# Kernel optimization log

Hardware: AMD Instinct MI355X
Metric: run time of the kernel (lower is better)

The kernel has to match this reference:

```python
import jax, jax.numpy as jnp
import numpy as np

B, V, C, H, W, D = 1, 3, 32, 320, 320, 32


def setup_inputs() -> dict:
    key = jax.random.key(0)
    ks = jax.random.split(key, 14)
    feats = jax.random.normal(ks[0], (B, V, C, H, W), jnp.float32)
    # Valid pinhole projections: P = [[K @ [R|t]], [0,0,0,1]], identity rotation,
    # horizontal baselines sized so the warp stays mostly in-image over the depth range.
    K = np.array([[400.0, 0.0, W / 2.0], [0.0, 400.0, H / 2.0], [0.0, 0.0, 1.0]])
    mats = []
    for tx in (0.0, 100.0, -100.0):
        Rt = np.eye(4)
        Rt[0, 3] = tx
        P = np.eye(4)
        P[:3, :4] = K @ Rt[:3, :4]
        mats.append(P)
    proj = jnp.asarray(np.broadcast_to(np.stack(mats)[None], (B, V, 4, 4)).copy(), jnp.float32)
    planes = jnp.linspace(425.0, 935.0, D, dtype=jnp.float32)
    depth_values = jnp.broadcast_to(planes[None, :, None, None], (B, D, H, W)).astype(jnp.float32)
    s = 0.05  # small init so exp(reg_cost) stays well-scaled
    W0 = s * jax.random.normal(ks[1], (8, C, 3, 3), jnp.float32)
    Ws1 = s * jax.random.normal(ks[2], (8, 8, 3, 3), jnp.float32)
    W1 = s * jax.random.normal(ks[3], (16, 8, 3, 3), jnp.float32)
    Ws2 = s * jax.random.normal(ks[4], (16, 16, 3, 3), jnp.float32)
    W2 = s * jax.random.normal(ks[5], (32, 16, 3, 3), jnp.float32)
    Ws3 = s * jax.random.normal(ks[6], (32, 32, 3, 3), jnp.float32)
    W3 = s * jax.random.normal(ks[7], (64, 32, 3, 3), jnp.float32)
    Ws4 = s * jax.random.normal(ks[8], (64, 64, 3, 3), jnp.float32)
    U4 = s * jax.random.normal(ks[9], (32, 64, 1, 1), jnp.float32)
    U3 = s * jax.random.normal(ks[10], (16, 32, 1, 1), jnp.float32)
    U2 = s * jax.random.normal(ks[11], (8, 16, 1, 1), jnp.float32)
    Wout = s * jax.random.normal(ks[12], (1, 8, 3, 3), jnp.float32)
    return dict(feats=feats, proj=proj, depth_values=depth_values, W0=W0, Ws1=Ws1,
                W1=W1, Ws2=Ws2, W2=W2, Ws3=Ws3, W3=W3, Ws4=Ws4, U4=U4, U3=U3, U2=U2, Wout=Wout)


def _conv(x, w, stride=1):
    return jax.lax.conv_general_dilated(x, w, (stride, stride), 'SAME',
                                        dimension_numbers=('NCHW', 'OIHW', 'NCHW'))


def _up2(x):
    return jnp.repeat(jnp.repeat(x, 2, axis=2), 2, axis=3)


def _bilinear(img, x, y):
    # img [C,H,W]; x,y [N] pixel coords; zero padding, align_corners semantics
    Cc, Hh, Ww = img.shape
    x0 = jnp.floor(x)
    y0 = jnp.floor(y)
    wx = x - x0
    wy = y - y0

    def tap(xi, yi):
        valid = ((xi >= 0) & (xi <= Ww - 1) & (yi >= 0) & (yi <= Hh - 1)).astype(img.dtype)
        xc = jnp.clip(xi, 0, Ww - 1).astype(jnp.int32)
        yc = jnp.clip(yi, 0, Hh - 1).astype(jnp.int32)
        return img[:, yc, xc] * valid  # [C,N]

    return (tap(x0, y0) * (1 - wx) * (1 - wy) + tap(x0 + 1, y0) * wx * (1 - wy)
            + tap(x0, y0 + 1) * (1 - wx) * wy + tap(x0 + 1, y0 + 1) * wx * wy)


def _forward(feats, proj, depth_values, W0, Ws1, W1, Ws2, W2, Ws3, W3, Ws4, U4, U3, U2, Wout):
    Bn, Vn, Cn, Hn, Wn = feats.shape
    Dn = depth_values.shape[1]
    N = Hn * Wn
    relu = jax.nn.relu
    ref = feats[:, 0]
    ref_sq = ref * ref
    # Precompute per-src-view rotated pixel rays and translations.
    inv_ref = jnp.linalg.inv(proj[:, 0])                       # [B,4,4]
    rel = jnp.einsum('bvij,bjk->bvik', proj[:, 1:], inv_ref)   # [B,V-1,4,4]
    rot, trans = rel[:, :, :3, :3], rel[:, :, :3, 3]
    ys, xs = jnp.meshgrid(jnp.arange(Hn), jnp.arange(Wn), indexing='ij')
    pix = jnp.stack([xs.ravel(), ys.ravel(), jnp.ones(N)], 0).astype(feats.dtype)  # [3,N]
    rot_pix = jnp.einsum('bvij,jn->bvin', rot, pix)            # [B,V-1,3,N]

    def regularize(x, s1, s2, s3, s4):
        c1 = relu(_conv(x, W0) + _conv(s1, Ws1))
        c2 = relu(_conv(c1, W1, 2) + _conv(s2, Ws2))
        c3 = relu(_conv(c2, W2, 2) + _conv(s3, Ws3))
        c4 = relu(_conv(c3, W3, 2) + _conv(s4, Ws4))
        u3 = c3 + _up2(_conv(c4, U4))
        u2 = c2 + _up2(_conv(u3, U3))
        u1 = c1 + _up2(_conv(u2, U2))
        return _conv(u1, Wout), c1, c2, c3, c4

    def step(carry, depth_slice):  # depth_slice [B,H,W]
        s1, s2, s3, s4, exp_sum, depth_img, max_prob = carry
        vol_sum, vol_sq = ref, ref_sq
        dflat = depth_slice.reshape(Bn, 1, N)
        for v in range(Vn - 1):
            xyz = rot_pix[:, v] * dflat + trans[:, v, :, None]   # [B,3,N]
            px = xyz[:, 0] / xyz[:, 2]
            py = xyz[:, 1] / xyz[:, 2]
            warped = jax.vmap(_bilinear)(feats[:, v + 1], px, py).reshape(Bn, Cn, Hn, Wn)
            vol_sum = vol_sum + warped
            vol_sq = vol_sq + warped * warped
        variance = vol_sq / Vn - (vol_sum / Vn) ** 2
        cost, s1, s2, s3, s4 = regularize(variance, s1, s2, s3, s4)
        prob = jnp.exp(cost)                                     # [B,1,H,W]
        max_prob = jnp.maximum(max_prob, prob)                   # == flag*prob + (1-flag)*max
        depth_img = depth_img + depth_slice[:, None] * prob
        exp_sum = exp_sum + prob
        return (s1, s2, s3, s4, exp_sum, depth_img, max_prob), None

    z = lambda c, h, w: jnp.zeros((Bn, c, h, w), feats.dtype)
    init = (z(8, Hn, Wn), z(16, Hn // 2, Wn // 2), z(32, Hn // 4, Wn // 4), z(64, Hn // 8, Wn // 8),
            z(1, Hn, Wn), z(1, Hn, Wn), z(1, Hn, Wn))
    carry, _ = jax.lax.scan(step, init, jnp.moveaxis(depth_values, 1, 0))
    _, _, _, _, exp_sum, depth_img, max_prob = carry
    es = exp_sum + 1e-10
    depth_map = (depth_img / es)[:, 0]
    prob_map = (max_prob / es)[:, 0]
    return jnp.stack([depth_map, prob_map], axis=1)  # [B,2,H,W]


def reference(feats, proj, depth_values, W0, Ws1, W1, Ws2, W2, Ws3, W3, Ws4, U4, U3, U2, Wout):
    return _forward(feats, proj, depth_values, W0, Ws1, W1, Ws2, W2, Ws3, W3, Ws4, U4, U3, U2, Wout)
```

## Files before the change

### kernel.cpp

```cpp
#include <hip/hip_runtime.h>
#include <hip/hip_bf16.h>
#include <math.h>

#define HH 320
#define WW 320
#define NP (HH*WW)
#define CC 32
#define DD 32

#define H2 160
#define W2 160
#define N2 (H2*W2)
#define H4 80
#define W4 80
#define N4 (H4*W4)
#define H8 40
#define W8 40
#define N8 (H8*W8)

#define HALO 18
#define NHALO (HALO*HALO)

#define C1SZ (8*NP)
#define C2SZ (16*N2)
#define C3SZ (32*N4)
#define C4SZ (64*N8)

#define SMEM_FLOATS (32*36 + 16*100 + 8*NHALO)

#define OFF_REL   0
#define OFF_C1R   64
#define OFF_C2R   (OFF_C1R + 5*C1SZ)
#define OFF_C3R   (OFF_C2R + 4*C2SZ)
#define OFF_C4R   (OFF_C3R + 3*C3SZ)
#define OFF_ESUM  (OFF_C4R + 2*C4SZ)
#define OFF_DIMG  (OFF_ESUM + NP)
#define OFF_MAXP  (OFF_DIMG + NP)
#define OFF_END   (OFF_MAXP + NP)

__global__ void k_prep(const float* __restrict__ proj, float* __restrict__ rel) {
    if (threadIdx.x != 0 || blockIdx.x != 0) return;
    double a[4][8];
    for (int i = 0; i < 4; i++)
        for (int j = 0; j < 4; j++) {
            a[i][j] = (double)proj[i*4 + j];
            a[i][j+4] = (i == j) ? 1.0 : 0.0;
        }
    for (int c = 0; c < 4; c++) {
        int pv = c; double best = fabs(a[c][c]);
        for (int r = c+1; r < 4; r++) {
            double v = fabs(a[r][c]);
            if (v > best) { best = v; pv = r; }
        }
        if (pv != c)
            for (int j = 0; j < 8; j++) { double t = a[c][j]; a[c][j] = a[pv][j]; a[pv][j] = t; }
        double inv = 1.0 / a[c][c];
        for (int j = 0; j < 8; j++) a[c][j] *= inv;
        for (int r = 0; r < 4; r++) if (r != c) {
            double f = a[r][c];
            for (int j = 0; j < 8; j++) a[r][j] -= f * a[c][j];
        }
    }
    for (int v = 1; v < 3; v++) {
        const float* P = proj + v*16;
        double rm[4][4];
        for (int i = 0; i < 4; i++)
            for (int j = 0; j < 4; j++) {
                double s = 0.0;
                for (int k = 0; k < 4; k++) s += (double)P[i*4 + k] * a[k][j+4];
                rm[i][j] = s;
            }
        float* o = rel + (v-1)*12;
        o[0]=(float)rm[0][0]; o[1]=(float)rm[0][1]; o[2]=(float)rm[0][2];
        o[3]=(float)rm[1][0]; o[4]=(float)rm[1][1]; o[5]=(float)rm[1][2];
        o[6]=(float)rm[2][0]; o[7]=(float)rm[2][1]; o[8]=(float)rm[2][2];
        o[9]=(float)rm[0][3]; o[10]=(float)rm[1][3]; o[11]=(float)rm[2][3];
    }
}


__device__ void stageA(int blk, int d,
        const float* __restrict__ feats, const float* __restrict__ rel,
        const float* __restrict__ depthv, const float* __restrict__ c1r,
        const float* __restrict__ W0, const float* __restrict__ Ws1,
        float* buf) {
    const float* dslice = depthv + (size_t)d * NP;
    const float* s1 = c1r + (size_t)((d+4)%5) * C1SZ;
    float* c1out = (float*)c1r + (size_t)(d%5) * C1SZ;

    int bx = blk % 20, by = blk / 20;
    int ox0 = bx*16, oy0 = by*16;

    const float* f1 = feats + CC*NP;
    const float* f2 = feats + 2*CC*NP;
    const float inv3 = 1.0f / 3.0f;

    int opx = threadIdx.x & 15, opy = threadIdx.x >> 4;
    int obase = opy*HALO + opx;
    int outp = (oy0 + opy)*WW + ox0 + opx;

    float acc[8];
#pragma unroll
    for (int o = 0; o < 8; o++) acc[o] = 0.0f;

    for (int chunk = 0; chunk < 4; chunk++) {
        int cbase = chunk*8;
        for (int hp = threadIdx.x; hp < NHALO; hp += 256) {
            int hy = hp / HALO, hx = hp - hy*HALO;
            int gy = oy0 + hy - 1, gx = ox0 + hx - 1;
            if (gy < 0 || gy >= HH || gx < 0 || gx >= WW) {
#pragma unroll
                for (int c = 0; c < 8; c++) buf[c*NHALO + hp] = 0.0f;
            } else {
                int p = gy*WW + gx;
                float depth = dslice[p];
                float fx = (float)gx, fy = (float)gy;
                int offs[8]; float wts[8];
#pragma unroll
                for (int v = 0; v < 2; v++) {
                    const float* r = rel + v*12;
                    float X = (r[0]*fx + r[1]*fy + r[2]) * depth + r[9];
                    float Y = (r[3]*fx + r[4]*fy + r[5]) * depth + r[10];
                    float Z = (r[6]*fx + r[7]*fy + r[8]) * depth + r[11];
                    float iz = 1.0f / Z;
                    float px = X * iz, py = Y * iz;
                    float x0f = floorf(px), y0f = floorf(py);
                    float wx = px - x0f, wy = py - y0f;
                    int x0 = (int)x0f, y0 = (int)y0f;
#pragma unroll
                    for (int t = 0; t < 4; t++) {
                        int xi = x0 + (t & 1), yi = y0 + (t >> 1);
                        float wgt = ((t & 1) ? wx : 1.0f - wx) * ((t >> 1) ? wy : 1.0f - wy);
                        bool valid = (xi >= 0) && (xi <= WW-1) && (yi >= 0) && (yi <= HH-1);
                        int xc = min(max(xi, 0), WW-1);
                        int yc = min(max(yi, 0), HH-1);
                        offs[v*4 + t] = yc*WW + xc;
                        wts[v*4 + t] = valid ? wgt : 0.0f;
                    }
                }
#pragma unroll
                for (int c = 0; c < 8; c++) {
                    int cg = cbase + c;
                    float rv = feats[cg*NP + p];
                    float sum = rv, sq = rv * rv;
                    const float* b1 = f1 + cg*NP;
                    float t1 = b1[offs[0]]*wts[0] + b1[offs[1]]*wts[1] + b1[offs[2]]*wts[2] + b1[offs[3]]*wts[3];
                    const float* b2 = f2 + cg*NP;
                    float t2 = b2[offs[4]]*wts[4] + b2[offs[5]]*wts[5] + b2[offs[6]]*wts[6] + b2[offs[7]]*wts[7];
                    sum += t1 + t2;
                    sq  += t1*t1 + t2*t2;
                    float m = sum * inv3;
                    buf[c*NHALO + hp] = sq * inv3 - m*m;
                }
            }
        }
        __syncthreads();
        for (int ci = 0; ci < 8; ci++) {
            float t[9];
#pragma unroll
            for (int ky = 0; ky < 3; ky++)
#pragma unroll
                for (int kx = 0; kx < 3; kx++) t[ky*3+kx] = buf[ci*NHALO + obase + ky*HALO + kx];
#pragma unroll
            for (int o = 0; o < 8; o++) {
                const float* w = W0 + (o*32 + cbase + ci)*9;
                float a = acc[o];
#pragma unroll
                for (int k = 0; k < 9; k++) a += t[k] * w[k];
                acc[o] = a;
            }
        }
        __syncthreads();
    }

    for (int hp = threadIdx.x; hp < NHALO; hp += 256) {
        int hy = hp / HALO, hx = hp - hy*HALO;
        int gy = oy0 + hy - 1, gx = ox0 + hx - 1;
        bool v = (gy >= 0) && (gy < HH) && (gx >= 0) && (gx < WW);
        int p = v ? gy*WW + gx : 0;
#pragma unroll
        for (int c = 0; c < 8; c++) buf[c*NHALO + hp] = v ? s1[c*NP + p] : 0.0f;
    }
    __syncthreads();
    for (int ci = 0; ci < 8; ci++) {
        float t[9];
#pragma unroll
        for (int ky = 0; ky < 3; ky++)
#pragma unroll
            for (int kx = 0; kx < 3; kx++) t[ky*3+kx] = buf[ci*NHALO + obase + ky*HALO + kx];
#pragma unroll
        for (int o = 0; o < 8; o++) {
            const float* w = Ws1 + (o*8 + ci)*9;
            float a = acc[o];
#pragma unroll
            for (int k = 0; k < 9; k++) a += t[k] * w[k];
            acc[o] = a;
        }
    }
#pragma unroll
    for (int o = 0; o < 8; o++) c1out[o*NP + outp] = fmaxf(acc[o], 0.0f);
}

__device__ void stageB(int blk, int d,
        const float* __restrict__ c1r, const float* __restrict__ c2r_,
        const float* __restrict__ W1, const float* __restrict__ Ws2) {
    const float* c1 = c1r + (size_t)(d%5) * C1SZ;
    const float* s2 = c2r_ + (size_t)((d+3)%4) * C2SZ;
    float* c2 = (float*)c2r_ + (size_t)(d%4) * C2SZ;
    int p = (blk % 100)*256 + threadIdx.x;
    if (p >= N2) return;
    int og = blk / 100;
    int y = p / W2, x = p - y*W2;
    int offsA[9]; float mskA[9];
#pragma unroll
    for (int k = 0; k < 9; k++) {
        int yy = 2*y + k/3, xx = 2*x + k%3;
        bool v = (yy < HH) && (xx < WW);
        offsA[k] = v ? yy*WW + xx : 0;
        mskA[k] = v ? 1.0f : 0.0f;
    }
    int offsB[9]; float mskB[9];
#pragma unroll
    for (int k = 0; k < 9; k++) {
        int yy = y + k/3 - 1, xx = x + k%3 - 1;
        bool v = (yy >= 0) && (yy < H2) && (xx >= 0) && (xx < W2);
        offsB[k] = v ? yy*W2 + xx : 0;
        mskB[k] = v ? 1.0f : 0.0f;
    }
    float acc[4];
#pragma unroll
    for (int o = 0; o < 4; o++) acc[o] = 0.0f;
    for (int ci = 0; ci < 8; ci++) {
        const float* b = c1 + ci*NP;
        float t[9];
#pragma unroll
        for (int k = 0; k < 9; k++) t[k] = b[offsA[k]] * mskA[k];
#pragma unroll
        for (int o = 0; o < 4; o++) {
            const float* w = W1 + ((og*4 + o)*8 + ci)*9;
            float a = acc[o];
#pragma unroll
            for (int k = 0; k < 9; k++) a += t[k] * w[k];
            acc[o] = a;
        }
    }
    for (int ci = 0; ci < 16; ci++) {
        const float* b = s2 + ci*N2;
        float t[9];
#pragma unroll
        for (int k = 0; k < 9; k++) t[k] = b[offsB[k]] * mskB[k];
#pragma unroll
        for (int o = 0; o < 4; o++) {
            const float* w = Ws2 + ((og*4 + o)*16 + ci)*9;
            float a = acc[o];
#pragma unroll
            for (int k = 0; k < 9; k++) a += t[k] * w[k];
            acc[o] = a;
        }
    }
#pragma unroll
    for (int o = 0; o < 4; o++) c2[(og*4 + o)*N2 + p] = fmaxf(acc[o], 0.0f);
}

__device__ void stageC(int blk, int d,
        const float* __restrict__ c2r_, const float* __restrict__ c3r_,
        const float* __restrict__ W2w, const float* __restrict__ Ws3) {
    const float* c2 = c2r_ + (size_t)(d%4) * C2SZ;
    const float* s3 = c3r_ + (size_t)((d+2)%3) * C3SZ;
    float* c3 = (float*)c3r_ + (size_t)(d%3) * C3SZ;
    int p = (blk % 25)*256 + threadIdx.x;
    if (p >= N4) return;
    int og = blk / 25;
    int y = p / W4, x = p - y*W4;
    int offsA[9]; float mskA[9];
#pragma unroll
    for (int k = 0; k < 9; k++) {
        int yy = 2*y + k/3, xx = 2*x + k%3;
        bool v = (yy < H2) && (xx < W2);
        offsA[k] = v ? yy*W2 + xx : 0;
        mskA[k] = v ? 1.0f : 0.0f;
    }
    int offsB[9]; float mskB[9];
#pragma unroll
    for (int k = 0; k < 9; k++) {
        int yy = y + k/3 - 1, xx = x + k%3 - 1;
        bool v = (yy >= 0) && (yy < H4) && (xx >= 0) && (xx < W4);
        offsB[k] = v ? yy*W4 + xx : 0;
        mskB[k] = v ? 1.0f : 0.0f;
    }
    float acc[4];
#pragma unroll
    for (int o = 0; o < 4; o++) acc[o] = 0.0f;
    for (int ci = 0; ci < 16; ci++) {
        const float* b = c2 + ci*N2;
        float t[9];
#pragma unroll
        for (int k = 0; k < 9; k++) t[k] = b[offsA[k]] * mskA[k];
#pragma unroll
        for (int o = 0; o < 4; o++) {
            const float* w = W2w + ((og*4 + o)*16 + ci)*9;
            float a = acc[o];
#pragma unroll
            for (int k = 0; k < 9; k++) a += t[k] * w[k];
            acc[o] = a;
        }
    }
    for (int ci = 0; ci < 32; ci++) {
        const float* b = s3 + ci*N4;
        float t[9];
#pragma unroll
        for (int k = 0; k < 9; k++) t[k] = b[offsB[k]] * mskB[k];
#pragma unroll
        for (int o = 0; o < 4; o++) {
            const float* w = Ws3 + ((og*4 + o)*32 + ci)*9;
            float a = acc[o];
#pragma unroll
            for (int k = 0; k < 9; k++) a += t[k] * w[k];
            acc[o] = a;
        }
    }
#pragma unroll
    for (int o = 0; o < 4; o++) c3[(og*4 + o)*N4 + p] = fmaxf(acc[o], 0.0f);
}

__device__ void stageD(int blk, int d,
        const float* __restrict__ c3r_, const float* __restrict__ c4r_,
        const float* __restrict__ W3w, const float* __restrict__ Ws4) {
    const float* c3 = c3r_ + (size_t)(d%3) * C3SZ;
    const float* s4 = c4r_ + (size_t)((d+1)%2) * C4SZ;
    float* c4 = (float*)c4r_ + (size_t)(d%2) * C4SZ;
    int p = (blk % 7)*256 + threadIdx.x;
    if (p >= N8) return;
    int og = blk / 7;
    int y = p / W8, x = p - y*W8;
    int offsA[9]; float mskA[9];
#pragma unroll
    for (int k = 0; k < 9; k++) {
        int yy = 2*y + k/3, xx = 2*x + k%3;
        bool v = (yy < H4) && (xx < W4);
        offsA[k] = v ? yy*W4 + xx : 0;
        mskA[k] = v ? 1.0f : 0.0f;
    }
    int offsB[9]; float mskB[9];
#pragma unroll
    for (int k = 0; k < 9; k++) {
        int yy = y + k/3 - 1, xx = x + k%3 - 1;
        bool v = (yy >= 0) && (yy < H8) && (xx >= 0) && (xx < W8);
        offsB[k] = v ? yy*W8 + xx : 0;
        mskB[k] = v ? 1.0f : 0.0f;
    }
    float acc[4];
#pragma unroll
    for (int o = 0; o < 4; o++) acc[o] = 0.0f;
    for (int ci = 0; ci < 32; ci++) {
        const float* b = c3 + ci*N4;
        float t[9];
#pragma unroll
        for (int k = 0; k < 9; k++) t[k] = b[offsA[k]] * mskA[k];
#pragma unroll
        for (int o = 0; o < 4; o++) {
            const float* w = W3w + ((og*4 + o)*32 + ci)*9;
            float a = acc[o];
#pragma unroll
            for (int k = 0; k < 9; k++) a += t[k] * w[k];
            acc[o] = a;
        }
    }
    for (int ci = 0; ci < 64; ci++) {
        const float* b = s4 + ci*N8;
        float t[9];
#pragma unroll
        for (int k = 0; k < 9; k++) t[k] = b[offsB[k]] * mskB[k];
#pragma unroll
        for (int o = 0; o < 4; o++) {
            const float* w = Ws4 + ((og*4 + o)*64 + ci)*9;
            float a = acc[o];
#pragma unroll
            for (int k = 0; k < 9; k++) a += t[k] * w[k];
            acc[o] = a;
        }
    }
#pragma unroll
    for (int o = 0; o < 4; o++) c4[(og*4 + o)*N8 + p] = fmaxf(acc[o], 0.0f);
}

__device__ void stageU(int blk, int d,
        const float* __restrict__ c1r, const float* __restrict__ c2r_,
        const float* __restrict__ c3r_, const float* __restrict__ c4r_,
        const float* __restrict__ U4, const float* __restrict__ U3,
        const float* __restrict__ U2, const float* __restrict__ Wout,
        const float* __restrict__ depthv,
        float* __restrict__ exp_sum, float* __restrict__ depth_img,
        float* __restrict__ max_prob, float* smem) {
    const float* c1 = c1r + (size_t)(d%5) * C1SZ;
    const float* c2 = c2r_ + (size_t)(d%4) * C2SZ;
    const float* c3 = c3r_ + (size_t)(d%3) * C3SZ;
    const float* c4 = c4r_ + (size_t)(d%2) * C4SZ;
    const float* dslice = depthv + (size_t)d * NP;
    float* u3s = smem;
    float* u2s = smem + 32*36;
    float* u1s = smem + 32*36 + 16*100;

    int bx = blk % 20, by = blk / 20;
    int ox0 = bx*16, oy0 = by*16;
    int qy0 = (oy0 >> 2) - 1, qx0 = (ox0 >> 2) - 1;
    int hy0 = (oy0 >> 1) - 1, hx0 = (ox0 >> 1) - 1;

    for (int i = threadIdx.x; i < 32*36; i += 256) {
        int ch = i / 36, pp = i - ch*36;
        int y4 = qy0 + pp/6, x4 = qx0 + pp%6;
        int y4c = min(max(y4, 0), H4-1), x4c = min(max(x4, 0), W4-1);
        int pl = (y4c >> 1)*W8 + (x4c >> 1);
        const float* w = U4 + ch*64;
        float s = c3[ch*N4 + y4c*W4 + x4c];
#pragma unroll 8
        for (int ci = 0; ci < 64; ci++) s += c4[ci*N8 + pl] * w[ci];
        u3s[ch*36 + pp] = s;
    }
    __syncthreads();
    for (int i = threadIdx.x; i < 16*100; i += 256) {
        int ch = i / 100, pp = i - ch*100;
        int y2 = hy0 + pp/10, x2 = hx0 + pp%10;
        int y2c = min(max(y2, 0), H2-1), x2c = min(max(x2, 0), W2-1);
        int ly = (y2c >> 1) - qy0, lx = (x2c >> 1) - qx0;
        const float* w = U3 + ch*32;
        float s = c2[ch*N2 + y2c*W2 + x2c];
#pragma unroll 8
        for (int ci = 0; ci < 32; ci++) s += u3s[ci*36 + ly*6 + lx] * w[ci];
        u2s[ch*100 + pp] = s;
    }
    __syncthreads();
    for (int i = threadIdx.x; i < 8*NHALO; i += 256) {
        int ch = i / NHALO, pp = i - ch*NHALO;
        int gy = oy0 + pp/HALO - 1, gx = ox0 + pp%HALO - 1;
        float s = 0.0f;
        if (gy >= 0 && gy < HH && gx >= 0 && gx < WW) {
            int ly = (gy >> 1) - hy0, lx = (gx >> 1) - hx0;
            const float* w = U2 + ch*16;
            s = c1[ch*NP + gy*WW + gx];
#pragma unroll
            for (int ci = 0; ci < 16; ci++) s += u2s[ci*100 + ly*10 + lx] * w[ci];
        }
        u1s[ch*NHALO + pp] = s;
    }
    __syncthreads();
    int px = threadIdx.x & 15, py = threadIdx.x >> 4;
    int base = py*HALO + px;
    float cost = 0.0f;
#pragma unroll
    for (int ci = 0; ci < 8; ci++) {
        const float* w = Wout + ci*9;
#pragma unroll
        for (int ky = 0; ky < 3; ky++)
#pragma unroll
            for (int kx = 0; kx < 3; kx++)
                cost += u1s[ci*NHALO + base + ky*HALO + kx] * w[ky*3 + kx];
    }
    int p = (oy0 + py)*WW + ox0 + px;
    float prob = expf(cost);
    exp_sum[p] += prob;
    depth_img[p] += dslice[p] * prob;
    max_prob[p] = fmaxf(max_prob[p], prob);
}

__global__ __launch_bounds__(256) void k_uber(
        int t,
        const float* __restrict__ feats, const float* __restrict__ rel,
        const float* __restrict__ depthv,
        const float* __restrict__ W0, const float* __restrict__ Ws1,
        const float* __restrict__ W1, const float* __restrict__ Ws2,
        const float* __restrict__ W2w, const float* __restrict__ Ws3,
        const float* __restrict__ W3w, const float* __restrict__ Ws4,
        const float* __restrict__ U4, const float* __restrict__ U3,
        const float* __restrict__ U2, const float* __restrict__ Wout,
        float* __restrict__ c1r, float* __restrict__ c2r,
        float* __restrict__ c3r, float* __restrict__ c4r,
        float* __restrict__ esum, float* __restrict__ dimg,
        float* __restrict__ maxp) {
    __shared__ float smem[SMEM_FLOATS];
    int b = blockIdx.x;
    if (b < 400) {
        int d = t;
        if (d < DD) stageA(b, d, feats, rel, depthv, c1r, W0, Ws1, smem);
    } else if (b < 800) {
        int d = t - 1;
        if (d >= 0 && d < DD) stageB(b - 400, d, c1r, c2r, W1, Ws2);
    } else if (b < 1000) {
        int d = t - 2;
        if (d >= 0 && d < DD) stageC(b - 800, d, c2r, c3r, W2w, Ws3);
    } else if (b < 1112) {
        int d = t - 3;
        if (d >= 0 && d < DD) stageD(b - 1000, d, c3r, c4r, W3w, Ws4);
    } else {
        int d = t - 4;
        if (d >= 0 && d < DD)
            stageU(b - 1112, d, c1r, c2r, c3r, c4r, U4, U3, U2, Wout, depthv,
                   esum, dimg, maxp, smem);
    }
}

__global__ __launch_bounds__(256) void k_final(
        const float* __restrict__ exp_sum, const float* __restrict__ depth_img,
        const float* __restrict__ max_prob, float* __restrict__ out) {
    int p = blockIdx.x*256 + threadIdx.x;
    if (p >= NP) return;
    float es = exp_sum[p] + 1e-10f;
    out[p] = depth_img[p] / es;
    out[NP + p] = max_prob[p] / es;
}

extern "C" void kernel_launch(void* const* d_in, const int* in_sizes, int n_in,
                              void* d_out, int out_size, void* d_ws, size_t ws_size,
                              hipStream_t stream) {
    const float* feats = (const float*)d_in[0];
    const float* proj  = (const float*)d_in[1];
    const float* depthv= (const float*)d_in[2];
    const float* W0  = (const float*)d_in[3];
    const float* Ws1 = (const float*)d_in[4];
    const float* W1  = (const float*)d_in[5];
    const float* Ws2 = (const float*)d_in[6];
    const float* W2w = (const float*)d_in[7];
    const float* Ws3 = (const float*)d_in[8];
    const float* W3w = (const float*)d_in[9];
    const float* Ws4 = (const float*)d_in[10];
    const float* U4  = (const float*)d_in[11];
    const float* U3  = (const float*)d_in[12];
    const float* U2  = (const float*)d_in[13];
    const float* Wout= (const float*)d_in[14];

    float* ws = (float*)d_ws;
    float* rel  = ws + OFF_REL;
    float* c1r  = ws + OFF_C1R;
    float* c2r  = ws + OFF_C2R;
    float* c3r  = ws + OFF_C3R;
    float* c4r  = ws + OFF_C4R;
    float* esum = ws + OFF_ESUM;
    float* dimg = ws + OFF_DIMG;
    float* maxp = ws + OFF_MAXP;

    hipMemsetAsync(c1r, 0, (size_t)(OFF_END - OFF_C1R) * sizeof(float), stream);
    k_prep<<<1, 1, 0, stream>>>(proj, rel);

    for (int t = 0; t < DD + 4; t++) {
        k_uber<<<dim3(1512), 256, 0, stream>>>(t, feats, rel, depthv,
            W0, Ws1, W1, Ws2, W2w, Ws3, W3w, Ws4, U4, U3, U2, Wout,
            c1r, c2r, c3r, c4r, esum, dimg, maxp);
    }
    k_final<<<dim3(400), 256, 0, stream>>>(esum, dimg, maxp, (float*)d_out);
}
```

Baseline: 2.994 ms.

## Convert features to fp16 channels-last and retile all stages to NHWC with 128-thread blocks

Precomputes a channels-last fp16 copy of the input features so each bilinear tap loads 8 channels in one vector load instead of strided fp32 gathers. All intermediate activation ring buffers switch to pixel-major NHWC layout with float4 loads and stores. Blocks shrink to 128 threads over 16x8 tiles, which doubles the grid, and smem is padded to avoid bank conflicts. The fp16 features add rounding error to the variance cost volume, and the different reduction order may shift results slightly.

```diff
diff --git a/kernel.cpp b/kernel.cpp
--- a/kernel.cpp
+++ b/kernel.cpp
@@ -1,5 +1,6 @@
 #include <hip/hip_runtime.h>
 #include <hip/hip_bf16.h>
+#include <hip/hip_fp16.h>
 #include <math.h>
 
 #define HH 320
@@ -7,7 +8,6 @@
 #define NP (HH*WW)
 #define CC 32
 #define DD 32
-
 #define H2 160
 #define W2 160
 #define N2 (H2*W2)
@@ -18,25 +18,55 @@
 #define W8 40
 #define N8 (H8*W8)
 
-#define HALO 18
-#define NHALO (HALO*HALO)
+#define AHW 18
+#define AHH 10
+#define ANH (AHW*AHH)
+#define ABUF_STRIDE 184
+
+#define U3_PX 24
+#define U3_STRIDE 33
+#define U2_PX 60
+#define U2_STRIDE 17
+#define U1_PX 180
+#define U1_STRIDE 9
+
+#define SMEM_FLOATS (U3_PX*U3_STRIDE + U2_PX*U2_STRIDE + U1_PX*U1_STRIDE)
 
 #define C1SZ (8*NP)
 #define C2SZ (16*N2)
 #define C3SZ (32*N4)
 #define C4SZ (64*N8)
 
-#define SMEM_FLOATS (32*36 + 16*100 + 8*NHALO)
-
-#define OFF_REL   0
-#define OFF_C1R   64
-#define OFF_C2R   (OFF_C1R + 5*C1SZ)
-#define OFF_C3R   (OFF_C2R + 4*C2SZ)
-#define OFF_C4R   (OFF_C3R + 3*C3SZ)
-#define OFF_ESUM  (OFF_C4R + 2*C4SZ)
-#define OFF_DIMG  (OFF_ESUM + NP)
-#define OFF_MAXP  (OFF_DIMG + NP)
-#define OFF_END   (OFF_MAXP + NP)
+#define OFF_REL  0
+#define OFF_FH   64
+#define FH_FLOATS (3*NP*32/2)
+#define OFF_C1R  (OFF_FH + FH_FLOATS)
+#define OFF_C2R  (OFF_C1R + 5*C1SZ)
+#define OFF_C3R  (OFF_C2R + 4*C2SZ)
+#define OFF_C4R  (OFF_C3R + 3*C3SZ)
+#define OFF_ESUM (OFF_C4R + 2*C4SZ)
+#define OFF_DIMG (OFF_ESUM + NP)
+#define OFF_MAXP (OFF_DIMG + NP)
+#define OFF_END  (OFF_MAXP + NP)
+
+#define A_END 800
+#define B_END 1600
+#define C_END 2000
+#define D_END 2208
+#define TOT_BLK 3008
+
+__device__ __forceinline__ void load8h(const __half* b, float o[8]) {
+    float4 f = *reinterpret_cast<const float4*>(b);
+    const __half2* h = reinterpret_cast<const __half2*>(&f);
+#pragma unroll
+    for (int j = 0; j < 4; j++) { float2 t = __half22float2(h[j]); o[2*j] = t.x; o[2*j+1] = t.y; }
+}
+__device__ __forceinline__ void load8f(const float* b, float o[8]) {
+    float4 x = reinterpret_cast<const float4*>(b)[0];
+    float4 y = reinterpret_cast<const float4*>(b)[1];
+    o[0]=x.x; o[1]=x.y; o[2]=x.z; o[3]=x.w; o[4]=y.x; o[5]=y.y; o[6]=y.z; o[7]=y.w;
+}
+__device__ __forceinline__ void load16f(const float* b, float o[16]) { load8f(b,o); load8f(b+8,o+8); }
 
 __global__ void k_prep(const float* __restrict__ proj, float* __restrict__ rel) {
     if (threadIdx.x != 0 || blockIdx.x != 0) return;
@@ -78,44 +108,48 @@
     }
 }
 
+__global__ __launch_bounds__(256) void k_tofp16(const float* __restrict__ feats,
+                                                __half* __restrict__ fh) {
+    int i = blockIdx.x*256 + threadIdx.x;
+    if (i >= 3*NP) return;
+    int v = i / NP, p = i - v*NP;
+    const float* src = feats + (size_t)v*CC*NP + p;
+    union { __half h[32]; float4 f4[4]; } u;
+#pragma unroll
+    for (int c = 0; c < 32; c++) u.h[c] = __float2half(src[(size_t)c*NP]);
+    float4* dst = (float4*)(fh + (size_t)i*32);
+#pragma unroll
+    for (int q = 0; q < 4; q++) dst[q] = u.f4[q];
+}
+
 
 __device__ void stageA(int blk, int d,
-        const float* __restrict__ feats, const float* __restrict__ rel,
-        const float* __restrict__ depthv, const float* __restrict__ c1r,
+        const __half* __restrict__ fh, const float* __restrict__ rel,
+        const float* __restrict__ depthv, float* __restrict__ c1r,
         const float* __restrict__ W0, const float* __restrict__ Ws1,
         float* buf) {
-    const float* dslice = depthv + (size_t)d * NP;
-    const float* s1 = c1r + (size_t)((d+4)%5) * C1SZ;
-    float* c1out = (float*)c1r + (size_t)(d%5) * C1SZ;
-
+    const float* s1 = c1r + (size_t)((d+4)%5)*C1SZ;
+    float* c1out = c1r + (size_t)(d%5)*C1SZ;
     int bx = blk % 20, by = blk / 20;
-    int ox0 = bx*16, oy0 = by*16;
-
-    const float* f1 = feats + CC*NP;
-    const float* f2 = feats + 2*CC*NP;
-    const float inv3 = 1.0f / 3.0f;
-
-    int opx = threadIdx.x & 15, opy = threadIdx.x >> 4;
-    int obase = opy*HALO + opx;
-    int outp = (oy0 + opy)*WW + ox0 + opx;
-
-    float acc[8];
-#pragma unroll
-    for (int o = 0; o < 8; o++) acc[o] = 0.0f;
-
-    for (int chunk = 0; chunk < 4; chunk++) {
-        int cbase = chunk*8;
-        for (int hp = threadIdx.x; hp < NHALO; hp += 256) {
-            int hy = hp / HALO, hx = hp - hy*HALO;
+    int ox0 = bx*16, oy0 = by*8;
+    int tid = threadIdx.x;
+
+    int ppix[2]; bool inimg[2];
+    int pls[2][8]; float wts[2][8];
+#pragma unroll
+    for (int j = 0; j < 2; j++) {
+        int hp = tid + j*128;
+        inimg[j] = false; ppix[j] = 0;
+#pragma unroll
+        for (int t = 0; t < 8; t++) { pls[j][t] = 0; wts[j][t] = 0.0f; }
+        if (hp < ANH) {
+            int hy = hp / AHW, hx = hp - hy*AHW;
             int gy = oy0 + hy - 1, gx = ox0 + hx - 1;
-            if (gy < 0 || gy >= HH || gx < 0 || gx >= WW) {
-#pragma unroll
-                for (int c = 0; c < 8; c++) buf[c*NHALO + hp] = 0.0f;
-            } else {
-                int p = gy*WW + gx;
-                float depth = dslice[p];
+            if (gy >= 0 && gy < HH && gx >= 0 && gx < WW) {
+                inimg[j] = true;
+                int p = gy*WW + gx; ppix[j] = p;
+                float depth = depthv[(size_t)d*NP + p];
                 float fx = (float)gx, fy = (float)gy;
-                int offs[8]; float wts[8];
 #pragma unroll
                 for (int v = 0; v < 2; v++) {
                     const float* r = rel + v*12;
@@ -123,35 +157,69 @@
                     float Y = (r[3]*fx + r[4]*fy + r[5]) * depth + r[10];
                     float Z = (r[6]*fx + r[7]*fy + r[8]) * depth + r[11];
                     float iz = 1.0f / Z;
-                    float px = X * iz, py = Y * iz;
+                    float px = X*iz, py = Y*iz;
                     float x0f = floorf(px), y0f = floorf(py);
                     float wx = px - x0f, wy = py - y0f;
                     int x0 = (int)x0f, y0 = (int)y0f;
 #pragma unroll
                     for (int t = 0; t < 4; t++) {
-                        int xi = x0 + (t & 1), yi = y0 + (t >> 1);
-                        float wgt = ((t & 1) ? wx : 1.0f - wx) * ((t >> 1) ? wy : 1.0f - wy);
-                        bool valid = (xi >= 0) && (xi <= WW-1) && (yi >= 0) && (yi <= HH-1);
-                        int xc = min(max(xi, 0), WW-1);
-                        int yc = min(max(yi, 0), HH-1);
-                        offs[v*4 + t] = yc*WW + xc;
-                        wts[v*4 + t] = valid ? wgt : 0.0f;
+                        int xi = x0 + (t&1), yi = y0 + (t>>1);
+                        float wgt = ((t&1)?wx:1.0f-wx) * ((t>>1)?wy:1.0f-wy);
+                        bool val = (xi>=0)&&(xi<WW)&&(yi>=0)&&(yi<HH);
+                        int xc = min(max(xi,0),WW-1), yc = min(max(yi,0),HH-1);
+                        pls[j][v*4+t] = yc*WW + xc;
+                        wts[j][v*4+t] = val ? wgt : 0.0f;
                     }
                 }
-#pragma unroll
-                for (int c = 0; c < 8; c++) {
-                    int cg = cbase + c;
-                    float rv = feats[cg*NP + p];
-                    float sum = rv, sq = rv * rv;
-                    const float* b1 = f1 + cg*NP;
-                    float t1 = b1[offs[0]]*wts[0] + b1[offs[1]]*wts[1] + b1[offs[2]]*wts[2] + b1[offs[3]]*wts[3];
-                    const float* b2 = f2 + cg*NP;
-                    float t2 = b2[offs[4]]*wts[4] + b2[offs[5]]*wts[5] + b2[offs[6]]*wts[6] + b2[offs[7]]*wts[7];
-                    sum += t1 + t2;
-                    sq  += t1*t1 + t2*t2;
-                    float m = sum * inv3;
-                    buf[c*NHALO + hp] = sq * inv3 - m*m;
-                }
+            }
+        }
+    }
+
+    int opx = tid & 15, opy = tid >> 4;
+    float acc[8];
+#pragma unroll
+    for (int o = 0; o < 8; o++) acc[o] = 0.0f;
+    const float inv3 = 1.0f/3.0f;
+
+    for (int chunk = 0; chunk < 4; chunk++) {
+        int c0 = chunk*8;
+#pragma unroll
+        for (int j = 0; j < 2; j++) {
+            int hp = tid + j*128;
+            if (hp < ANH) {
+                float out8[8];
+                if (!inimg[j]) {
+#pragma unroll
+                    for (int c = 0; c < 8; c++) out8[c] = 0.0f;
+                } else {
+                    float ref8[8]; load8h(fh + ((size_t)ppix[j]*32 + c0), ref8);
+                    float t1[8], t2[8];
+#pragma unroll
+                    for (int c = 0; c < 8; c++) { t1[c] = 0.0f; t2[c] = 0.0f; }
+#pragma unroll
+                    for (int t = 0; t < 4; t++) {
+                        float tap[8]; load8h(fh + ((size_t)(NP + pls[j][t])*32 + c0), tap);
+                        float w = wts[j][t];
+#pragma unroll
+                        for (int c = 0; c < 8; c++) t1[c] += tap[c]*w;
+                    }
+#pragma unroll
+                    for (int t = 0; t < 4; t++) {
+                        float tap[8]; load8h(fh + ((size_t)(2*NP + pls[j][4+t])*32 + c0), tap);
+                        float w = wts[j][4+t];
+#pragma unroll
+                        for (int c = 0; c < 8; c++) t2[c] += tap[c]*w;
+                    }
+#pragma unroll
+                    for (int c = 0; c < 8; c++) {
+                        float sum = ref8[c] + t1[c] + t2[c];
+                        float sq  = ref8[c]*ref8[c] + t1[c]*t1[c] + t2[c]*t2[c];
+                        float m = sum*inv3;
+                        out8[c] = sq*inv3 - m*m;
+                    }
+                }
+#pragma unroll
+                for (int c = 0; c < 8; c++) buf[c*ABUF_STRIDE + hp] = out8[c];
             }
         }
         __syncthreads();
@@ -160,26 +228,30 @@
 #pragma unroll
             for (int ky = 0; ky < 3; ky++)
 #pragma unroll
-                for (int kx = 0; kx < 3; kx++) t[ky*3+kx] = buf[ci*NHALO + obase + ky*HALO + kx];
+                for (int kx = 0; kx < 3; kx++)
+                    t[ky*3+kx] = buf[ci*ABUF_STRIDE + (opy+ky)*AHW + opx + kx];
 #pragma unroll
             for (int o = 0; o < 8; o++) {
-                const float* w = W0 + (o*32 + cbase + ci)*9;
+                const float* w = W0 + (o*32 + c0 + ci)*9;
                 float a = acc[o];
 #pragma unroll
-                for (int k = 0; k < 9; k++) a += t[k] * w[k];
+                for (int k = 0; k < 9; k++) a += t[k]*w[k];
                 acc[o] = a;
             }
         }
         __syncthreads();
     }
 
-    for (int hp = threadIdx.x; hp < NHALO; hp += 256) {
-        int hy = hp / HALO, hx = hp - hy*HALO;
-        int gy = oy0 + hy - 1, gx = ox0 + hx - 1;
-        bool v = (gy >= 0) && (gy < HH) && (gx >= 0) && (gx < WW);
-        int p = v ? gy*WW + gx : 0;
-#pragma unroll
-        for (int c = 0; c < 8; c++) buf[c*NHALO + hp] = v ? s1[c*NP + p] : 0.0f;
+#pragma unroll
+    for (int j = 0; j < 2; j++) {
+        int hp = tid + j*128;
+        if (hp < ANH) {
+            float v8[8];
+            if (inimg[j]) load8f(s1 + (size_t)ppix[j]*8, v8);
+            else { for (int c = 0; c < 8; c++) v8[c] = 0.0f; }
+#pragma unroll
+            for (int c = 0; c < 8; c++) buf[c*ABUF_STRIDE + hp] = v8[c];
+        }
     }
     __syncthreads();
     for (int ci = 0; ci < 8; ci++) {
@@ -187,285 +259,280 @@
 #pragma unroll
         for (int ky = 0; ky < 3; ky++)
 #pragma unroll
-            for (int kx = 0; kx < 3; kx++) t[ky*3+kx] = buf[ci*NHALO + obase + ky*HALO + kx];
+            for (int kx = 0; kx < 3; kx++)
+                t[ky*3+kx] = buf[ci*ABUF_STRIDE + (opy+ky)*AHW + opx + kx];
 #pragma unroll
         for (int o = 0; o < 8; o++) {
             const float* w = Ws1 + (o*8 + ci)*9;
             float a = acc[o];
 #pragma unroll
-            for (int k = 0; k < 9; k++) a += t[k] * w[k];
+            for (int k = 0; k < 9; k++) a += t[k]*w[k];
             acc[o] = a;
         }
     }
-#pragma unroll
-    for (int o = 0; o < 8; o++) c1out[o*NP + outp] = fmaxf(acc[o], 0.0f);
+    int outp = (oy0 + opy)*WW + ox0 + opx;
+    float4 r0, r1;
+    r0.x = fmaxf(acc[0],0.0f); r0.y = fmaxf(acc[1],0.0f); r0.z = fmaxf(acc[2],0.0f); r0.w = fmaxf(acc[3],0.0f);
+    r1.x = fmaxf(acc[4],0.0f); r1.y = fmaxf(acc[5],0.0f); r1.z = fmaxf(acc[6],0.0f); r1.w = fmaxf(acc[7],0.0f);
+    float4* dst = (float4*)(c1out + (size_t)outp*8);
+    dst[0] = r0; dst[1] = r1;
 }
 
 __device__ void stageB(int blk, int d,
-        const float* __restrict__ c1r, const float* __restrict__ c2r_,
+        const float* __restrict__ c1r, float* __restrict__ c2r,
         const float* __restrict__ W1, const float* __restrict__ Ws2) {
-    const float* c1 = c1r + (size_t)(d%5) * C1SZ;
-    const float* s2 = c2r_ + (size_t)((d+3)%4) * C2SZ;
-    float* c2 = (float*)c2r_ + (size_t)(d%4) * C2SZ;
-    int p = (blk % 100)*256 + threadIdx.x;
-    if (p >= N2) return;
-    int og = blk / 100;
+    const float* c1 = c1r + (size_t)(d%5)*C1SZ;
+    const float* s2 = c2r + (size_t)((d+3)%4)*C2SZ;
+    float* c2 = c2r + (size_t)(d%4)*C2SZ;
+    int p = (blk % 200)*128 + threadIdx.x;
+    int og = blk / 200;
     int y = p / W2, x = p - y*W2;
-    int offsA[9]; float mskA[9];
-#pragma unroll
-    for (int k = 0; k < 9; k++) {
-        int yy = 2*y + k/3, xx = 2*x + k%3;
-        bool v = (yy < HH) && (xx < WW);
-        offsA[k] = v ? yy*WW + xx : 0;
-        mskA[k] = v ? 1.0f : 0.0f;
-    }
-    int offsB[9]; float mskB[9];
-#pragma unroll
-    for (int k = 0; k < 9; k++) {
-        int yy = y + k/3 - 1, xx = x + k%3 - 1;
-        bool v = (yy >= 0) && (yy < H2) && (xx >= 0) && (xx < W2);
-        offsB[k] = v ? yy*W2 + xx : 0;
-        mskB[k] = v ? 1.0f : 0.0f;
-    }
-    float acc[4];
-#pragma unroll
-    for (int o = 0; o < 4; o++) acc[o] = 0.0f;
-    for (int ci = 0; ci < 8; ci++) {
-        const float* b = c1 + ci*NP;
-        float t[9];
-#pragma unroll
-        for (int k = 0; k < 9; k++) t[k] = b[offsA[k]] * mskA[k];
-#pragma unroll
-        for (int o = 0; o < 4; o++) {
-            const float* w = W1 + ((og*4 + o)*8 + ci)*9;
-            float a = acc[o];
-#pragma unroll
-            for (int k = 0; k < 9; k++) a += t[k] * w[k];
-            acc[o] = a;
-        }
-    }
-    for (int ci = 0; ci < 16; ci++) {
-        const float* b = s2 + ci*N2;
-        float t[9];
-#pragma unroll
-        for (int k = 0; k < 9; k++) t[k] = b[offsB[k]] * mskB[k];
-#pragma unroll
-        for (int o = 0; o < 4; o++) {
-            const float* w = Ws2 + ((og*4 + o)*16 + ci)*9;
-            float a = acc[o];
-#pragma unroll
-            for (int k = 0; k < 9; k++) a += t[k] * w[k];
-            acc[o] = a;
-        }
-    }
-#pragma unroll
-    for (int o = 0; o < 4; o++) c2[(og*4 + o)*N2 + p] = fmaxf(acc[o], 0.0f);
+    float acc[4] = {0.0f,0.0f,0.0f,0.0f};
+#pragma unroll
+    for (int ky = 0; ky < 3; ky++) {
+#pragma unroll
+        for (int kx = 0; kx < 3; kx++) {
+            int k = ky*3+kx;
+            int yy = 2*y+ky, xx = 2*x+kx;
+            if (yy < HH && xx < WW) {
+                float v8[8]; load8f(c1 + (size_t)(yy*WW+xx)*8, v8);
+#pragma unroll
+                for (int o = 0; o < 4; o++) {
+                    const float* w = W1 + ((og*4+o)*8)*9 + k;
+                    float a = acc[o];
+#pragma unroll
+                    for (int ci = 0; ci < 8; ci++) a += v8[ci]*w[ci*9];
+                    acc[o] = a;
+                }
+            }
+        }
+    }
+#pragma unroll
+    for (int ky = 0; ky < 3; ky++) {
+#pragma unroll
+        for (int kx = 0; kx < 3; kx++) {
+            int k = ky*3+kx;
+            int yy = y+ky-1, xx = x+kx-1;
+            if (yy >= 0 && yy < H2 && xx >= 0 && xx < W2) {
+                float v16[16]; load16f(s2 + (size_t)(yy*W2+xx)*16, v16);
+#pragma unroll
+                for (int o = 0; o < 4; o++) {
+                    const float* w = Ws2 + ((og*4+o)*16)*9 + k;
+                    float a = acc[o];
+#pragma unroll
+                    for (int ci = 0; ci < 16; ci++) a += v16[ci]*w[ci*9];
+                    acc[o] = a;
+                }
+            }
+        }
+    }
+    float4 r;
+    r.x = fmaxf(acc[0],0.0f); r.y = fmaxf(acc[1],0.0f); r.z = fmaxf(acc[2],0.0f); r.w = fmaxf(acc[3],0.0f);
+    *((float4*)(c2 + (size_t)p*16 + og*4)) = r;
 }
 
 __device__ void stageC(int blk, int d,
-        const float* __restrict__ c2r_, const float* __restrict__ c3r_,
+        const float* __restrict__ c2r, float* __restrict__ c3r,
         const float* __restrict__ W2w, const float* __restrict__ Ws3) {
-    const float* c2 = c2r_ + (size_t)(d%4) * C2SZ;
-    const float* s3 = c3r_ + (size_t)((d+2)%3) * C3SZ;
-    float* c3 = (float*)c3r_ + (size_t)(d%3) * C3SZ;
-    int p = (blk % 25)*256 + threadIdx.x;
-    if (p >= N4) return;
-    int og = blk / 25;
+    const float* c2 = c2r + (size_t)(d%4)*C2SZ;
+    const float* s3 = c3r + (size_t)((d+2)%3)*C3SZ;
+    float* c3 = c3r + (size_t)(d%3)*C3SZ;
+    int p = (blk % 50)*128 + threadIdx.x;
+    int og = blk / 50;
     int y = p / W4, x = p - y*W4;
-    int offsA[9]; float mskA[9];
-#pragma unroll
-    for (int k = 0; k < 9; k++) {
-        int yy = 2*y + k/3, xx = 2*x + k%3;
-        bool v = (yy < H2) && (xx < W2);
-        offsA[k] = v ? yy*W2 + xx : 0;
-        mskA[k] = v ? 1.0f : 0.0f;
-    }
-    int offsB[9]; float mskB[9];
-#pragma unroll
-    for (int k = 0; k < 9; k++) {
-        int yy = y + k/3 - 1, xx = x + k%3 - 1;
-        bool v = (yy >= 0) && (yy < H4) && (xx >= 0) && (xx < W4);
-        offsB[k] = v ? yy*W4 + xx : 0;
-        mskB[k] = v ? 1.0f : 0.0f;
-    }
-    float acc[4];
-#pragma unroll
-    for (int o = 0; o < 4; o++) acc[o] = 0.0f;
-    for (int ci = 0; ci < 16; ci++) {
-        const float* b = c2 + ci*N2;
-        float t[9];
-#pragma unroll
-        for (int k = 0; k < 9; k++) t[k] = b[offsA[k]] * mskA[k];
-#pragma unroll
-        for (int o = 0; o < 4; o++) {
-            const float* w = W2w + ((og*4 + o)*16 + ci)*9;
-            float a = acc[o];
-#pragma unroll
-            for (int k = 0; k < 9; k++) a += t[k] * w[k];
-            acc[o] = a;
-        }
-    }
-    for (int ci = 0; ci < 32; ci++) {
-        const float* b = s3 + ci*N4;
-        float t[9];
-#pragma unroll
-        for (int k = 0; k < 9; k++) t[k] = b[offsB[k]] * mskB[k];
-#pragma unroll
-        for (int o = 0; o < 4; o++) {
-            const float* w = Ws3 + ((og*4 + o)*32 + ci)*9;
-            float a = acc[o];
-#pragma unroll
-            for (int k = 0; k < 9; k++) a += t[k] * w[k];
-            acc[o] = a;
-        }
-    }
-#pragma unroll
-    for (int o = 0; o < 4; o++) c3[(og*4 + o)*N4 + p] = fmaxf(acc[o], 0.0f);
+    float acc[4] = {0.0f,0.0f,0.0f,0.0f};
+#pragma unroll
+    for (int ky = 0; ky < 3; ky++) {
+#pragma unroll
+        for (int kx = 0; kx < 3; kx++) {
+            int k = ky*3+kx;
+            int yy = 2*y+ky, xx = 2*x+kx;
+            if (yy < H2 && xx < W2) {
+                float v16[16]; load16f(c2 + (size_t)(yy*W2+xx)*16, v16);
+#pragma unroll
+                for (int o = 0; o < 4; o++) {
+                    const float* w = W2w + ((og*4+o)*16)*9 + k;
+                    float a = acc[o];
+#pragma unroll
+                    for (int ci = 0; ci < 16; ci++) a += v16[ci]*w[ci*9];
+                    acc[o] = a;
+                }
+            }
+        }
+    }
+#pragma unroll
+    for (int ky = 0; ky < 3; ky++) {
+#pragma unroll
+        for (int kx = 0; kx < 3; kx++) {
+            int k = ky*3+kx;
+            int yy = y+ky-1, xx = x+kx-1;
+            if (yy >= 0 && yy < H4 && xx >= 0 && xx < W4) {
+                const float4* b = (const float4*)(s3 + (size_t)(yy*W4+xx)*32);
+#pragma unroll
+                for (int q = 0; q < 8; q++) {
+                    float4 v = b[q];
+#pragma unroll
+                    for (int o = 0; o < 4; o++) {
+                        const float* w = Ws3 + ((og*4+o)*32 + q*4)*9 + k;
+                        acc[o] += v.x*w[0] + v.y*w[9] + v.z*w[18] + v.w*w[27];
+                    }
+                }
+            }
+        }
+    }
+    float4 r;
+    r.x = fmaxf(acc[0],0.0f); r.y = fmaxf(acc[1],0.0f); r.z = fmaxf(acc[2],0.0f); r.w = fmaxf(acc[3],0.0f);
+    *((float4*)(c3 + (size_t)p*32 + og*4)) = r;
 }
 
 __device__ void stageD(int blk, int d,
-        const float* __restrict__ c3r_, const float* __restrict__ c4r_,
+        const float* __restrict__ c3r, float* __restrict__ c4r,
         const float* __restrict__ W3w, const float* __restrict__ Ws4) {
-    const float* c3 = c3r_ + (size_t)(d%3) * C3SZ;
-    const float* s4 = c4r_ + (size_t)((d+1)%2) * C4SZ;
-    float* c4 = (float*)c4r_ + (size_t)(d%2) * C4SZ;
-    int p = (blk % 7)*256 + threadIdx.x;
+    const float* c3 = c3r + (size_t)(d%3)*C3SZ;
+    const float* s4 = c4r + (size_t)((d+1)%2)*C4SZ;
+    float* c4 = c4r + (size_t)(d%2)*C4SZ;
+    int p = (blk % 13)*128 + threadIdx.x;
     if (p >= N8) return;
-    int og = blk / 7;
+    int og = blk / 13;
     int y = p / W8, x = p - y*W8;
-    int offsA[9]; float mskA[9];
-#pragma unroll
-    for (int k = 0; k < 9; k++) {
-        int yy = 2*y + k/3, xx = 2*x + k%3;
-        bool v = (yy < H4) && (xx < W4);
-        offsA[k] = v ? yy*W4 + xx : 0;
-        mskA[k] = v ? 1.0f : 0.0f;
-    }
-    int offsB[9]; float mskB[9];
-#pragma unroll
-    for (int k = 0; k < 9; k++) {
-        int yy = y + k/3 - 1, xx = x + k%3 - 1;
-        bool v = (yy >= 0) && (yy < H8) && (xx >= 0) && (xx < W8);
-        offsB[k] = v ? yy*W8 + xx : 0;
-        mskB[k] = v ? 1.0f : 0.0f;
-    }
-    float acc[4];
-#pragma unroll
-    for (int o = 0; o < 4; o++) acc[o] = 0.0f;
-    for (int ci = 0; ci < 32; ci++) {
-        const float* b = c3 + ci*N4;
-        float t[9];
-#pragma unroll
-        for (int k = 0; k < 9; k++) t[k] = b[offsA[k]] * mskA[k];
-#pragma unroll
-        for (int o = 0; o < 4; o++) {
-            const float* w = W3w + ((og*4 + o)*32 + ci)*9;
-            float a = acc[o];
-#pragma unroll
-            for (int k = 0; k < 9; k++) a += t[k] * w[k];
-            acc[o] = a;
-        }
-    }
-    for (int ci = 0; ci < 64; ci++) {
-        const float* b = s4 + ci*N8;
-        float t[9];
-#pragma unroll
-        for (int k = 0; k < 9; k++) t[k] = b[offsB[k]] * mskB[k];
-#pragma unroll
-        for (int o = 0; o < 4; o++) {
-            const float* w = Ws4 + ((og*4 + o)*64 + ci)*9;
-            float a = acc[o];
-#pragma unroll
-            for (int k = 0; k < 9; k++) a += t[k] * w[k];
-            acc[o] = a;
-        }
-    }
-#pragma unroll
-    for (int o = 0; o < 4; o++) c4[(og*4 + o)*N8 + p] = fmaxf(acc[o], 0.0f);
+    float acc[4] = {0.0f,0.0f,0.0f,0.0f};
+#pragma unroll
+    for (int ky = 0; ky < 3; ky++) {
+#pragma unroll
+        for (int kx = 0; kx < 3; kx++) {
+            int k = ky*3+kx;
+            int yy = 2*y+ky, xx = 2*x+kx;
+            if (yy < H4 && xx < W4) {
+                const float4* b = (const float4*)(c3 + (size_t)(yy*W4+xx)*32);
+#pragma unroll
+                for (int q = 0; q < 8; q++) {
+                    float4 v = b[q];
+#pragma unroll
+                    for (int o = 0; o < 4; o++) {
+                        const float* w = W3w + ((og*4+o)*32 + q*4)*9 + k;
+                        acc[o] += v.x*w[0] + v.y*w[9] + v.z*w[18] + v.w*w[27];
+                    }
+                }
+            }
+        }
+    }
+#pragma unroll
+    for (int ky = 0; ky < 3; ky++) {
+#pragma unroll
+        for (int kx = 0; kx < 3; kx++) {
+            int k = ky*3+kx;
+            int yy = y+ky-1, xx = x+kx-1;
+            if (yy >= 0 && yy < H8 && xx >= 0 && xx < W8) {
+                const float4* b = (const float4*)(s4 + (size_t)(yy*W8+xx)*64);
+#pragma unroll
+                for (int q = 0; q < 16; q++) {
+                    float4 v = b[q];
+#pragma unroll
+                    for (int o = 0; o < 4; o++) {
+                        const float* w = Ws4 + ((og*4+o)*64 + q*4)*9 + k;
+                        acc[o] += v.x*w[0] + v.y*w[9] + v.z*w[18] + v.w*w[27];
+                    }
+                }
+            }
+        }
+    }
+    float4 r;
+    r.x = fmaxf(acc[0],0.0f); r.y = fmaxf(acc[1],0.0f); r.z = fmaxf(acc[2],0.0f); r.w = fmaxf(acc[3],0.0f);
+    *((float4*)(c4 + (size_t)p*64 + og*4)) = r;
 }
 
 __device__ void stageU(int blk, int d,
-        const float* __restrict__ c1r, const float* __restrict__ c2r_,
-        const float* __restrict__ c3r_, const float* __restrict__ c4r_,
-        const float* __restrict__ U4, const float* __restrict__ U3,
-        const float* __restrict__ U2, const float* __restrict__ Wout,
+        const float* __restrict__ c1r, const float* __restrict__ c2r,
+        const float* __restrict__ c3r, const float* __restrict__ c4r,
+        const float* __restrict__ U4, const float* __restrict__ U3w,
+        const float* __restrict__ U2w, const float* __restrict__ Wout,
         const float* __restrict__ depthv,
-        float* __restrict__ exp_sum, float* __restrict__ depth_img,
-        float* __restrict__ max_prob, float* smem) {
-    const float* c1 = c1r + (size_t)(d%5) * C1SZ;
-    const float* c2 = c2r_ + (size_t)(d%4) * C2SZ;
-    const float* c3 = c3r_ + (size_t)(d%3) * C3SZ;
-    const float* c4 = c4r_ + (size_t)(d%2) * C4SZ;
-    const float* dslice = depthv + (size_t)d * NP;
+        float* __restrict__ esum, float* __restrict__ dimg,
+        float* __restrict__ maxp, float* smem) {
+    const float* c1 = c1r + (size_t)(d%5)*C1SZ;
+    const float* c2 = c2r + (size_t)(d%4)*C2SZ;
+    const float* c3 = c3r + (size_t)(d%3)*C3SZ;
+    const float* c4 = c4r + (size_t)(d%2)*C4SZ;
+    const float* dsl = depthv + (size_t)d*NP;
     float* u3s = smem;
-    float* u2s = smem + 32*36;
-    float* u1s = smem + 32*36 + 16*100;
-
+    float* u2s = smem + U3_PX*U3_STRIDE;
+    float* u1s = u2s + U2_PX*U2_STRIDE;
     int bx = blk % 20, by = blk / 20;
-    int ox0 = bx*16, oy0 = by*16;
-    int qy0 = (oy0 >> 2) - 1, qx0 = (ox0 >> 2) - 1;
-    int hy0 = (oy0 >> 1) - 1, hx0 = (ox0 >> 1) - 1;
-
-    for (int i = threadIdx.x; i < 32*36; i += 256) {
-        int ch = i / 36, pp = i - ch*36;
+    int x0 = bx*16, y0 = by*8;
+    int qx0 = (x0>>2) - 1, qy0 = (y0>>2) - 1;
+    int hx0 = (x0>>1) - 1, hy0 = (y0>>1) - 1;
+    int tid = threadIdx.x;
+
+    for (int i = tid; i < U3_PX*32; i += 128) {
+        int ch = i & 31, pp = i >> 5;
         int y4 = qy0 + pp/6, x4 = qx0 + pp%6;
-        int y4c = min(max(y4, 0), H4-1), x4c = min(max(x4, 0), W4-1);
-        int pl = (y4c >> 1)*W8 + (x4c >> 1);
+        int y4c = min(max(y4,0),H4-1), x4c = min(max(x4,0),W4-1);
+        int pl = (y4c>>1)*W8 + (x4c>>1);
         const float* w = U4 + ch*64;
-        float s = c3[ch*N4 + y4c*W4 + x4c];
+        const float* b = c4 + (size_t)pl*64;
+        float s = c3[(size_t)(y4c*W4+x4c)*32 + ch];
 #pragma unroll 8
-        for (int ci = 0; ci < 64; ci++) s += c4[ci*N8 + pl] * w[ci];
-        u3s[ch*36 + pp] = s;
+        for (int ci = 0; ci < 64; ci++) s += b[ci]*w[ci];
+        u3s[pp*U3_STRIDE + ch] = s;
     }
     __syncthreads();
-    for (int i = threadIdx.x; i < 16*100; i += 256) {
-        int ch = i / 100, pp = i - ch*100;
+    for (int i = tid; i < U2_PX*16; i += 128) {
+        int ch = i & 15, pp = i >> 4;
         int y2 = hy0 + pp/10, x2 = hx0 + pp%10;
-        int y2c = min(max(y2, 0), H2-1), x2c = min(max(x2, 0), W2-1);
-        int ly = (y2c >> 1) - qy0, lx = (x2c >> 1) - qx0;
-        const float* w = U3 + ch*32;
-        float s = c2[ch*N2 + y2c*W2 + x2c];
+        int y2c = min(max(y2,0),H2-1), x2c = min(max(x2,0),W2-1);
+        int ly = (y2c>>1)-qy0, lx = (x2c>>1)-qx0;
+        const float* w = U3w + ch*32;
+        const float* b = u3s + (ly*6+lx)*U3_STRIDE;
+        float s = c2[(size_t)(y2c*W2+x2c)*16 + ch];
 #pragma unroll 8
-        for (int ci = 0; ci < 32; ci++) s += u3s[ci*36 + ly*6 + lx] * w[ci];
-        u2s[ch*100 + pp] = s;
+        for (int ci = 0; ci < 32; ci++) s += b[ci]*w[ci];
+        u2s[pp*U2_STRIDE + ch] = s;
     }
     __syncthreads();
-    for (int i = threadIdx.x; i < 8*NHALO; i += 256) {
-        int ch = i / NHALO, pp = i - ch*NHALO;
-        int gy = oy0 + pp/HALO - 1, gx = ox0 + pp%HALO - 1;
-        float s = 0.0f;
-        if (gy >= 0 && gy < HH && gx >= 0 && gx < WW) {
-            int ly = (gy >> 1) - hy0, lx = (gx >> 1) - hx0;
-            const float* w = U2 + ch*16;
-            s = c1[ch*NP + gy*WW + gx];
-#pragma unroll
-            for (int ci = 0; ci < 16; ci++) s += u2s[ci*100 + ly*10 + lx] * w[ci];
-        }
-        u1s[ch*NHALO + pp] = s;
+#pragma unroll
+    for (int j = 0; j < 2; j++) {
+        int pp = tid + j*128;
+        if (pp < U1_PX) {
+            int gy = y0 + pp/AHW - 1, gx = x0 + pp%AHW - 1;
+            if (gy >= 0 && gy < HH && gx >= 0 && gx < WW) {
+                int ly = (gy>>1)-hy0, lx = (gx>>1)-hx0;
+                const float* b = u2s + (ly*10+lx)*U2_STRIDE;
+                float v8[8]; load8f(c1 + (size_t)(gy*WW+gx)*8, v8);
+#pragma unroll
+                for (int ch = 0; ch < 8; ch++) {
+                    const float* w = U2w + ch*16;
+                    float s = v8[ch];
+#pragma unroll
+                    for (int ci = 0; ci < 16; ci++) s += b[ci]*w[ci];
+                    u1s[pp*U1_STRIDE + ch] = s;
+                }
+            } else {
+#pragma unroll
+                for (int ch = 0; ch < 8; ch++) u1s[pp*U1_STRIDE + ch] = 0.0f;
+            }
+        }
     }
     __syncthreads();
-    int px = threadIdx.x & 15, py = threadIdx.x >> 4;
-    int base = py*HALO + px;
+    int opx = tid & 15, opy = tid >> 4;
     float cost = 0.0f;
 #pragma unroll
-    for (int ci = 0; ci < 8; ci++) {
-        const float* w = Wout + ci*9;
-#pragma unroll
-        for (int ky = 0; ky < 3; ky++)
-#pragma unroll
-            for (int kx = 0; kx < 3; kx++)
-                cost += u1s[ci*NHALO + base + ky*HALO + kx] * w[ky*3 + kx];
-    }
-    int p = (oy0 + py)*WW + ox0 + px;
+    for (int ky = 0; ky < 3; ky++)
+#pragma unroll
+        for (int kx = 0; kx < 3; kx++) {
+            const float* b = u1s + ((opy+ky)*AHW + opx+kx)*U1_STRIDE;
+#pragma unroll
+            for (int ch = 0; ch < 8; ch++) cost += b[ch]*Wout[ch*9 + ky*3+kx];
+        }
+    int p = (y0+opy)*WW + x0 + opx;
     float prob = expf(cost);
-    exp_sum[p] += prob;
-    depth_img[p] += dslice[p] * prob;
-    max_prob[p] = fmaxf(max_prob[p], prob);
-}
-
-__global__ __launch_bounds__(256) void k_uber(
+    esum[p] += prob;
+    dimg[p] += dsl[p]*prob;
+    maxp[p] = fmaxf(maxp[p], prob);
+}
+
+__global__ __launch_bounds__(128, 6) void k_uber(
         int t,
-        const float* __restrict__ feats, const float* __restrict__ rel,
+        const __half* __restrict__ fh, const float* __restrict__ rel,
         const float* __restrict__ depthv,
         const float* __restrict__ W0, const float* __restrict__ Ws1,
         const float* __restrict__ W1, const float* __restrict__ Ws2,
@@ -479,22 +546,22 @@
         float* __restrict__ maxp) {
     __shared__ float smem[SMEM_FLOATS];
     int b = blockIdx.x;
-    if (b < 400) {
+    if (b < A_END) {
         int d = t;
-        if (d < DD) stageA(b, d, feats, rel, depthv, c1r, W0, Ws1, smem);
-    } else if (b < 800) {
+        if (d < DD) stageA(b, d, fh, rel, depthv, c1r, W0, Ws1, smem);
+    } else if (b < B_END) {
         int d = t - 1;
-        if (d >= 0 && d < DD) stageB(b - 400, d, c1r, c2r, W1, Ws2);
-    } else if (b < 1000) {
+        if (d >= 0 && d < DD) stageB(b - A_END, d, c1r, c2r, W1, Ws2);
+    } else if (b < C_END) {
         int d = t - 2;
-        if (d >= 0 && d < DD) stageC(b - 800, d, c2r, c3r, W2w, Ws3);
-    } else if (b < 1112) {
+        if (d >= 0 && d < DD) stageC(b - B_END, d, c2r, c3r, W2w, Ws3);
+    } else if (b < D_END) {
         int d = t - 3;
-        if (d >= 0 && d < DD) stageD(b - 1000, d, c3r, c4r, W3w, Ws4);
+        if (d >= 0 && d < DD) stageD(b - C_END, d, c3r, c4r, W3w, Ws4);
     } else {
         int d = t - 4;
         if (d >= 0 && d < DD)
-            stageU(b - 1112, d, c1r, c2r, c3r, c4r, U4, U3, U2, Wout, depthv,
+            stageU(b - D_END, d, c1r, c2r, c3r, c4r, U4, U3, U2, Wout, depthv,
                    esum, dimg, maxp, smem);
     }
 }
@@ -530,6 +597,7 @@
 
     float* ws = (float*)d_ws;
     float* rel  = ws + OFF_REL;
+    __half* fh  = (__half*)(ws + OFF_FH);
     float* c1r  = ws + OFF_C1R;
     float* c2r  = ws + OFF_C2R;
     float* c3r  = ws + OFF_C3R;
@@ -540,9 +608,10 @@
 
     hipMemsetAsync(c1r, 0, (size_t)(OFF_END - OFF_C1R) * sizeof(float), stream);
     k_prep<<<1, 1, 0, stream>>>(proj, rel);
+    k_tofp16<<<dim3((3*NP + 255)/256), 256, 0, stream>>>(feats, fh);
 
     for (int t = 0; t < DD + 4; t++) {
-        k_uber<<<dim3(1512), 256, 0, stream>>>(t, feats, rel, depthv,
+        k_uber<<<dim3(TOT_BLK), 128, 0, stream>>>(t, fh, rel, depthv,
             W0, Ws1, W1, Ws2, W2w, Ws3, W3w, Ws4, U4, U3, U2, Wout,
             c1r, c2r, c3r, c4r, esum, dimg, maxp);
     }
```

Measured after the change: 3.707 ms. 1.24x slower.
